# Optimization experiments

Measured on AMD Instinct MI355X. Metric: run time of the kernel, lower is better.

## Reference

```python
import jax, jax.numpy as jnp
import numpy as np

V, D, T_MAX, H, L = 96, 128, 64, 8, 4
HD = D // H          # 16
FF = 4 * D           # 512
B, T = 4096, 64
EPS = 1e-5


def setup_inputs() -> dict:
    key = jax.random.key(0)
    ks = jax.random.split(key, 24)
    n = jax.random.normal
    inp = {
        'idx': jax.random.randint(ks[0], (B, T), 0, V),
        'targets': jax.random.randint(ks[1], (B, T), 0, V),
        'tok_emb': n(ks[2], (V, D), jnp.float32) * 0.02,
        'pos_emb': n(ks[3], (T_MAX, D), jnp.float32) * 0.02,
        # per-layer stacked params; weight layout follows torch Linear [out, in]
        'Wq': n(ks[4], (L, D, D), jnp.float32) * (1.0 / np.sqrt(D)),
        'Wk': n(ks[5], (L, D, D), jnp.float32) * (1.0 / np.sqrt(D)),
        'Wv': n(ks[6], (L, D, D), jnp.float32) * (1.0 / np.sqrt(D)),
        'Wo': n(ks[7], (L, D, D), jnp.float32) * (1.0 / np.sqrt(D)),
        'bo': jnp.zeros((L, D), jnp.float32),
        'ln1_g': jnp.ones((L, D), jnp.float32),
        'ln1_b': jnp.zeros((L, D), jnp.float32),
        'ln2_g': jnp.ones((L, D), jnp.float32),
        'ln2_b': jnp.zeros((L, D), jnp.float32),
        'W1': n(ks[8], (L, FF, D), jnp.float32) * (1.0 / np.sqrt(D)),
        'b1': jnp.zeros((L, FF), jnp.float32),
        'W2': n(ks[9], (L, D, FF), jnp.float32) * (1.0 / np.sqrt(FF)),
        'b2': jnp.zeros((L, D), jnp.float32),
        'lnf_g': jnp.ones((D,), jnp.float32),
        'lnf_b': jnp.zeros((D,), jnp.float32),
        'lm_b': jnp.zeros((V,), jnp.float32),
    }
    return inp


def _layernorm(x, g, b):
    mu = jnp.mean(x, axis=-1, keepdims=True)
    var = jnp.mean(jnp.square(x - mu), axis=-1, keepdims=True)
    return (x - mu) * jax.lax.rsqrt(var + EPS) * g + b


def reference(idx, targets, tok_emb, pos_emb, Wq, Wk, Wv, Wo, bo,
              ln1_g, ln1_b, ln2_g, ln2_b, W1, b1, W2, b2,
              lnf_g, lnf_b, lm_b):
    Bc, Tc = idx.shape
    x = tok_emb[idx] + pos_emb[:Tc]                      # [B,T,D]
    causal = jnp.tril(jnp.ones((Tc, Tc), bool))
    scale = HD ** -0.5
    for l in range(L):  # small fixed layer count
        xn = _layernorm(x, ln1_g[l], ln1_b[l])
        # per-head Linears are blocks of a single [D,D] matmul
        q = (xn @ Wq[l].T).reshape(Bc, Tc, H, HD)
        k = (xn @ Wk[l].T).reshape(Bc, Tc, H, HD)
        v = (xn @ Wv[l].T).reshape(Bc, Tc, H, HD)
        wei = jnp.einsum('bqhd,bkhd->bhqk', q, k) * scale
        wei = jnp.where(causal, wei, -jnp.inf)
        wei = jax.nn.softmax(wei, axis=-1)               # dropout = identity (eval)
        att = jnp.einsum('bhqk,bkhd->bqhd', wei, v).reshape(Bc, Tc, D)
        x = x + att @ Wo[l].T + bo[l]
        xn = _layernorm(x, ln2_g[l], ln2_b[l])
        h = jax.nn.gelu(xn @ W1[l].T + b1[l], approximate=False)
        x = x + h @ W2[l].T + b2[l]
    x = _layernorm(x, lnf_g, lnf_b)
    logits = x @ tok_emb.T + lm_b                        # tied weights
    logits = logits.reshape(Bc * Tc, V)
    logp = jax.nn.log_softmax(logits, axis=-1)
    loss = -jnp.mean(jnp.take_along_axis(logp, targets.reshape(-1, 1), axis=-1))
    return logits, loss
```

## Files before the change

kernel.cpp:

```cpp
#include <hip/hip_runtime.h>
#include <hip/hip_bf16.h>
#include <math.h>

#define NTHR 512

typedef __attribute__((ext_vector_type(8))) short bf16x8;
typedef __attribute__((ext_vector_type(4))) short bf16x4;
typedef __attribute__((ext_vector_type(4))) float f32x4;

#define MFMA32(a, b, c) __builtin_amdgcn_mfma_f32_16x16x32_bf16((a), (b), (c), 0, 0, 0)

#if defined(__has_builtin)
#if __has_builtin(__builtin_amdgcn_mfma_f32_16x16x16bf16_1k)
#define HAVE_MFMA16 1
#endif
#endif
#ifdef HAVE_MFMA16
#define MFMA16(a, b, c) __builtin_amdgcn_mfma_f32_16x16x16bf16_1k((a), (b), (c), 0, 0, 0)
#else
__device__ __forceinline__ f32x4 mfma16_fb(bf16x4 a, bf16x4 b, f32x4 c) {
  asm volatile("s_nop 1\n\tv_mfma_f32_16x16x16_bf16 %0, %1, %2, %0\n\ts_nop 7\n\ts_nop 7"
               : "+v"(c) : "v"(a), "v"(b));
  return c;
}
#define MFMA16(a, b, c) mfma16_fb((a), (b), (c))
#endif

#define WS_EMB 0
#define WS_WQ  12288
#define WS_WK  (WS_WQ + 65536)
#define WS_WV  (WS_WK + 65536)
#define WS_WO  (WS_WV + 65536)
#define WS_W1  (WS_WO + 65536)
#define WS_W2  (WS_W1 + 262144)
#define WS_END (WS_W2 + 262144)

__device__ __forceinline__ short f2bf(float f) {
  union { __hip_bfloat16 h; unsigned short s; } u;
  u.h = __float2bfloat16(f);
  return (short)u.s;
}
__device__ __forceinline__ bf16x4 pk4(f32x4 v) {
  bf16x4 r;
  r[0] = f2bf(v[0]); r[1] = f2bf(v[1]); r[2] = f2bf(v[2]); r[3] = f2bf(v[3]);
  return r;
}
__device__ __forceinline__ float gelu_tanh(float x) {
  float y = x * (0.7978845608f + 0.0356774081f * x * x);
  float sg = __builtin_amdgcn_rcpf(1.f + __expf(-2.f * y));
  return x * sg;
}

__global__ void prep_weights(const float* __restrict__ tok_emb,
                             const float* __restrict__ Wq, const float* __restrict__ Wk,
                             const float* __restrict__ Wv, const float* __restrict__ Wo,
                             const float* __restrict__ W1, const float* __restrict__ W2,
                             short* __restrict__ wsb) {
  int i = blockIdx.x * NTHR + threadIdx.x;
  if (i < 12288) {
    int n = i >> 7, k = i & 127;
    wsb[WS_EMB + (k >> 3) * 768 + n * 8 + (k & 7)] = f2bf(tok_emb[i]);
    return;
  }
  i -= 12288;
  if (i < 262144) {
    int tensor = i >> 16;
    int rem = i & 65535;
    int l = rem >> 14;
    int w = rem & 16383;
    int n = w >> 7, k = w & 127;
    const float* src = tensor == 0 ? Wq : tensor == 1 ? Wk : tensor == 2 ? Wv : Wo;
    wsb[WS_WQ + tensor * 65536 + l * 16384 + (k >> 3) * 1024 + n * 8 + (k & 7)] =
        f2bf(src[rem]);
    return;
  }
  i -= 262144;
  if (i < 262144) {
    int l = i >> 16;
    int w = i & 65535;
    int n = w >> 7, k = w & 127;
    wsb[WS_W1 + l * 65536 + (k >> 3) * 4096 + n * 8 + (k & 7)] = f2bf(W1[i]);
    return;
  }
  i -= 262144;
  if (i < 262144) {
    int l = i >> 16;
    int w = i & 65535;
    int n = w >> 9, k = w & 511;
    wsb[WS_W2 + l * 65536 + (k >> 3) * 1024 + n * 8 + (k & 7)] = f2bf(W2[i]);
  }
}

__device__ __forceinline__ void layernorm(const float* __restrict__ sXl,
                                          short* __restrict__ dstl,
                                          const float* __restrict__ g,
                                          const float* __restrict__ be, int tid) {
  int r = tid >> 3, t8 = tid & 7;
  const f32x4* row = (const f32x4*)(sXl + r * 132 + t8 * 16);
  f32x4 v[4];
  float s = 0.f, s2 = 0.f;
#pragma unroll
  for (int j = 0; j < 4; ++j) {
    v[j] = row[j];
#pragma unroll
    for (int c = 0; c < 4; ++c) { s += v[j][c]; s2 += v[j][c] * v[j][c]; }
  }
  s  += __shfl_xor(s, 1, 64);  s  += __shfl_xor(s, 2, 64);  s  += __shfl_xor(s, 4, 64);
  s2 += __shfl_xor(s2, 1, 64); s2 += __shfl_xor(s2, 2, 64); s2 += __shfl_xor(s2, 4, 64);
  float mean = s * 0.0078125f;
  float rs = rsqrtf(s2 * 0.0078125f - mean * mean + 1e-5f);
  const f32x4* gp = (const f32x4*)(g + t8 * 16);
  const f32x4* bp = (const f32x4*)(be + t8 * 16);
  bf16x4* dp = (bf16x4*)(dstl + r * 136 + t8 * 16);
#pragma unroll
  for (int j = 0; j < 4; ++j) {
    f32x4 gg = gp[j], bb = bp[j], o;
#pragma unroll
    for (int c = 0; c < 4; ++c) o[c] = (v[j][c] - mean) * rs * gg[c] + bb[c];
    dp[j] = pk4(o);
  }
}

__global__ __launch_bounds__(512, 2)
void lm_forward(const int* __restrict__ idx, const int* __restrict__ targets,
                const float* __restrict__ tok_emb, const float* __restrict__ pos_emb,
                const float* __restrict__ bo, const float* __restrict__ ln1_g,
                const float* __restrict__ ln1_b, const float* __restrict__ ln2_g,
                const float* __restrict__ ln2_b, const float* __restrict__ b1,
                const float* __restrict__ b2, const float* __restrict__ lnf_g,
                const float* __restrict__ lnf_b, const float* __restrict__ lm_b,
                const short* __restrict__ wsb, float* __restrict__ out,
                float* __restrict__ loss_part) {
  __shared__ __align__(16) char smem[118016];
  float* sX  = (float*)smem;
  short* sXn = (short*)(smem + 33792);
  char*  Rg  = smem + 51200;
  short* sQ  = (short*)Rg;
  short* sK  = (short*)(Rg + 17408);
  short* sVT = (short*)(Rg + 34816);
  short* sH  = (short*)Rg;
  float* sL  = (float*)Rg;
  float* sRed = (float*)(smem + 117760);

  const int b = blockIdx.x;
  const int tid = threadIdx.x;
  const int wave = tid >> 6;
  const int lane = tid & 63;
  const int lr = lane & 15;
  const int lg = lane >> 4;
  const f32x4 fz = {0.f, 0.f, 0.f, 0.f};

#pragma unroll
  for (int k = 0; k < 4; ++k) {
    int e = (tid + k * 512) * 4;
    int t = e >> 7, d = e & 127;
    f32x4 te = *(const f32x4*)(tok_emb + idx[b * 64 + t] * 128 + d);
    f32x4 pe = *(const f32x4*)(pos_emb + e);
    *(f32x4*)(sX + t * 132 + d) = te + pe;
  }
  __syncthreads();

#pragma unroll 1
  for (int l = 0; l < 4; ++l) {
    layernorm(sX, sXn, ln1_g + l * 128, ln1_b + l * 128, tid);
    __syncthreads();

    {
      const short* wq = wsb + WS_WQ + l * 16384;
      const short* wk = wsb + WS_WK + l * 16384;
      const short* wv = wsb + WS_WV + l * 16384;
      f32x4 aq[4], ak[4], av[4];
#pragma unroll
      for (int n = 0; n < 4; ++n) { aq[n] = fz; ak[n] = fz; av[n] = fz; }
#pragma unroll
      for (int ks = 0; ks < 4; ++ks) {
        bf16x8 xf[4];
#pragma unroll
        for (int n = 0; n < 4; ++n)
          xf[n] = *(const bf16x8*)(sXn + (n * 16 + lr) * 136 + ks * 32 + lg * 8);
        int wo_ = (ks * 4 + lg) * 1024 + (wave * 16 + lr) * 8;
        bf16x8 qf = *(const bf16x8*)(wq + wo_);
        bf16x8 kf = *(const bf16x8*)(wk + wo_);
        bf16x8 vf = *(const bf16x8*)(wv + wo_);
#pragma unroll
        for (int n = 0; n < 4; ++n) {
          aq[n] = MFMA32(qf, xf[n], aq[n]);
          ak[n] = MFMA32(kf, xf[n], ak[n]);
          av[n] = MFMA32(xf[n], vf, av[n]);
        }
      }
#pragma unroll
      for (int n = 0; n < 4; ++n) {
        *(bf16x4*)(sQ + (n * 16 + lr) * 136 + wave * 16 + lg * 4) = pk4(aq[n]);
        *(bf16x4*)(sK + (n * 16 + lr) * 136 + wave * 16 + lg * 4) = pk4(ak[n]);
        *(bf16x4*)(sVT + (wave * 16 + lr) * 72 + n * 16 + lg * 4) = pk4(av[n]);
      }
    }
    __syncthreads();

    {
      const int h = wave;
      f32x4 sc[4][4];
#pragma unroll
      for (int m = 0; m < 4; ++m)
#pragma unroll
        for (int n = 0; n < 4; ++n) sc[m][n] = fz;
      bf16x4 kf[4], qf[4];
#pragma unroll
      for (int m = 0; m < 4; ++m)
        kf[m] = *(const bf16x4*)(sK + (m * 16 + lr) * 136 + h * 16 + lg * 4);
#pragma unroll
      for (int n = 0; n < 4; ++n)
        qf[n] = *(const bf16x4*)(sQ + (n * 16 + lr) * 136 + h * 16 + lg * 4);
#pragma unroll
      for (int m = 0; m < 4; ++m)
#pragma unroll
        for (int n = 0; n < 4; ++n) sc[m][n] = MFMA16(kf[m], qf[n], sc[m][n]);

      bf16x4 pf[4][4];
#pragma unroll
      for (int n = 0; n < 4; ++n) {
        int qq = n * 16 + lr;
        float mx = -1e30f;
#pragma unroll
        for (int m = 0; m < 4; ++m)
#pragma unroll
          for (int r = 0; r < 4; ++r) {
            int kk = m * 16 + lg * 4 + r;
            float s = sc[m][n][r];
            if (kk > qq) s = -1e30f;
            sc[m][n][r] = s;
            mx = fmaxf(mx, s);
          }
        mx = fmaxf(mx, __shfl_xor(mx, 16, 64));
        mx = fmaxf(mx, __shfl_xor(mx, 32, 64));
        float sum = 0.f;
#pragma unroll
        for (int m = 0; m < 4; ++m)
#pragma unroll
          for (int r = 0; r < 4; ++r) {
            float p = __expf((sc[m][n][r] - mx) * 0.25f);
            sc[m][n][r] = p;
            sum += p;
          }
        sum += __shfl_xor(sum, 16, 64);
        sum += __shfl_xor(sum, 32, 64);
        float rinv = __builtin_amdgcn_rcpf(sum);
#pragma unroll
        for (int m = 0; m < 4; ++m) {
          f32x4 pv;
#pragma unroll
          for (int r = 0; r < 4; ++r) pv[r] = sc[m][n][r] * rinv;
          pf[m][n] = pk4(pv);
        }
      }
      f32x4 ao[4];
#pragma unroll
      for (int n = 0; n < 4; ++n) ao[n] = fz;
#pragma unroll
      for (int m = 0; m < 4; ++m) {
        bf16x4 vf = *(const bf16x4*)(sVT + (h * 16 + lr) * 72 + m * 16 + lg * 4);
#pragma unroll
        for (int n = 0; n < 4; ++n) ao[n] = MFMA16(vf, pf[m][n], ao[n]);
      }
#pragma unroll
      for (int n = 0; n < 4; ++n)
        *(bf16x4*)(sXn + (n * 16 + lr) * 136 + h * 16 + lg * 4) = pk4(ao[n]);
    }
    __syncthreads();

    {
      const short* wo = wsb + WS_WO + l * 16384;
      f32x4 ac[4];
#pragma unroll
      for (int n = 0; n < 4; ++n) ac[n] = fz;
#pragma unroll
      for (int ks = 0; ks < 4; ++ks) {
        bf16x8 wf = *(const bf16x8*)(wo + (ks * 4 + lg) * 1024 + (wave * 16 + lr) * 8);
#pragma unroll
        for (int n = 0; n < 4; ++n) {
          bf16x8 bfg = *(const bf16x8*)(sXn + (n * 16 + lr) * 136 + ks * 32 + lg * 8);
          ac[n] = MFMA32(wf, bfg, ac[n]);
        }
      }
      f32x4 bo4 = *(const f32x4*)(bo + l * 128 + wave * 16 + lg * 4);
#pragma unroll
      for (int n = 0; n < 4; ++n) {
        f32x4* px = (f32x4*)(sX + (n * 16 + lr) * 132 + wave * 16 + lg * 4);
        *px = *px + ac[n] + bo4;
      }
    }
    __syncthreads();

    layernorm(sX, sXn, ln2_g + l * 128, ln2_b + l * 128, tid);
    __syncthreads();

    {
      const short* w1 = wsb + WS_W1 + l * 65536;
      const short* w2 = wsb + WS_W2 + l * 65536;
      f32x4 a1[4][4];
#pragma unroll
      for (int g = 0; g < 4; ++g)
#pragma unroll
        for (int n = 0; n < 4; ++n) a1[g][n] = fz;
#pragma unroll
      for (int ks = 0; ks < 4; ++ks) {
        bf16x8 xf[4];
#pragma unroll
        for (int n = 0; n < 4; ++n)
          xf[n] = *(const bf16x8*)(sXn + (n * 16 + lr) * 136 + ks * 32 + lg * 8);
#pragma unroll
        for (int g = 0; g < 4; ++g) {
          bf16x8 wf = *(const bf16x8*)(w1 + (ks * 4 + lg) * 4096 +
                                       (wave * 64 + g * 16 + lr) * 8);
#pragma unroll
          for (int n = 0; n < 4; ++n) a1[g][n] = MFMA32(wf, xf[n], a1[g][n]);
        }
      }
#pragma unroll
      for (int g = 0; g < 4; ++g) {
        f32x4 b1v = *(const f32x4*)(b1 + l * 512 + wave * 64 + g * 16 + lg * 4);
#pragma unroll
        for (int n = 0; n < 4; ++n) {
          f32x4 hv;
#pragma unroll
          for (int r = 0; r < 4; ++r) hv[r] = gelu_tanh(a1[g][n][r] + b1v[r]);
          *(bf16x4*)(sH + (n * 16 + lr) * 520 + wave * 64 + g * 16 + lg * 4) = pk4(hv);
        }
      }
      __syncthreads();
      f32x4 a2[4];
#pragma unroll
      for (int n = 0; n < 4; ++n) a2[n] = fz;
#pragma unroll
      for (int ks = 0; ks < 16; ++ks) {
        bf16x8 wf = *(const bf16x8*)(w2 + (ks * 4 + lg) * 1024 + (wave * 16 + lr) * 8);
#pragma unroll
        for (int n = 0; n < 4; ++n) {
          bf16x8 hf = *(const bf16x8*)(sH + (n * 16 + lr) * 520 + ks * 32 + lg * 8);
          a2[n] = MFMA32(wf, hf, a2[n]);
        }
      }
      f32x4 b2v = *(const f32x4*)(b2 + l * 128 + wave * 16 + lg * 4);
#pragma unroll
      for (int n = 0; n < 4; ++n) {
        f32x4* px = (f32x4*)(sX + (n * 16 + lr) * 132 + wave * 16 + lg * 4);
        *px = *px + a2[n] + b2v;
      }
    }
    __syncthreads();
  }

  layernorm(sX, sXn, lnf_g, lnf_b, tid);
  __syncthreads();

  if (wave < 6) {
    f32x4 al[4];
#pragma unroll
    for (int n = 0; n < 4; ++n) al[n] = fz;
#pragma unroll
    for (int ks = 0; ks < 4; ++ks) {
      bf16x8 ef = *(const bf16x8*)(wsb + WS_EMB + (ks * 4 + lg) * 768 +
                                   (wave * 16 + lr) * 8);
#pragma unroll
      for (int n = 0; n < 4; ++n) {
        bf16x8 xf = *(const bf16x8*)(sXn + (n * 16 + lr) * 136 + ks * 32 + lg * 8);
        al[n] = MFMA32(ef, xf, al[n]);
      }
    }
    f32x4 lb = *(const f32x4*)(lm_b + wave * 16 + lg * 4);
#pragma unroll
    for (int n = 0; n < 4; ++n) {
      f32x4 v = al[n] + lb;
      int token = n * 16 + lr;
      *(f32x4*)(out + ((size_t)b * 64 + token) * 96 + wave * 16 + lg * 4) = v;
      *(f32x4*)(sL + token * 100 + wave * 16 + lg * 4) = v;
    }
  }
  __syncthreads();

  {
    int r = tid >> 3, t8 = tid & 7;
    const float* lrow = sL + r * 100 + t8 * 12;
    float mx = -1e30f;
#pragma unroll
    for (int j = 0; j < 12; ++j) mx = fmaxf(mx, lrow[j]);
    mx = fmaxf(mx, __shfl_xor(mx, 1, 64));
    mx = fmaxf(mx, __shfl_xor(mx, 2, 64));
    mx = fmaxf(mx, __shfl_xor(mx, 4, 64));
    float sum = 0.f;
#pragma unroll
    for (int j = 0; j < 12; ++j) sum += __expf(lrow[j] - mx);
    sum += __shfl_xor(sum, 1, 64);
    sum += __shfl_xor(sum, 2, 64);
    sum += __shfl_xor(sum, 4, 64);
    if (t8 == 0) {
      float lse = logf(sum) + mx;
      sRed[r] = lse - sL[r * 100 + targets[b * 64 + r]];
    }
  }
  __syncthreads();
  if (wave == 0) {
    float v = sRed[lane];
#pragma unroll
    for (int m = 32; m >= 1; m >>= 1) v += __shfl_xor(v, m, 64);
    if (lane == 0) loss_part[b] = v;
  }
}

__global__ void loss_reduce(const float* __restrict__ loss_part, float* __restrict__ out_loss) {
  __shared__ float red[256];
  int t = threadIdx.x;
  float s = 0.f;
  for (int i = t; i < 4096; i += 256) s += loss_part[i];
  red[t] = s;
  __syncthreads();
  for (int k = 128; k >= 1; k >>= 1) {
    if (t < k) red[t] += red[t + k];
    __syncthreads();
  }
  if (t == 0) out_loss[0] = red[0] * (1.f / 262144.f);
}

extern "C" void kernel_launch(void* const* d_in, const int* in_sizes, int n_in,
                              void* d_out, int out_size, void* d_ws, size_t ws_size,
                              hipStream_t stream) {
  (void)in_sizes; (void)n_in; (void)ws_size;
  const int* idx      = (const int*)d_in[0];
  const int* targets  = (const int*)d_in[1];
  const float* tok_emb = (const float*)d_in[2];
  const float* pos_emb = (const float*)d_in[3];
  const float* Wq = (const float*)d_in[4];
  const float* Wk = (const float*)d_in[5];
  const float* Wv = (const float*)d_in[6];
  const float* Wo = (const float*)d_in[7];
  const float* bo = (const float*)d_in[8];
  const float* ln1_g = (const float*)d_in[9];
  const float* ln1_b = (const float*)d_in[10];
  const float* ln2_g = (const float*)d_in[11];
  const float* ln2_b = (const float*)d_in[12];
  const float* W1 = (const float*)d_in[13];
  const float* b1 = (const float*)d_in[14];
  const float* W2 = (const float*)d_in[15];
  const float* b2 = (const float*)d_in[16];
  const float* lnf_g = (const float*)d_in[17];
  const float* lnf_b = (const float*)d_in[18];
  const float* lm_b = (const float*)d_in[19];

  short* wsb = (short*)d_ws;
  float* loss_part = (float*)((char*)d_ws + (size_t)WS_END * 2);
  float* out = (float*)d_out;

  prep_weights<<<1560, NTHR, 0, stream>>>(tok_emb, Wq, Wk, Wv, Wo, W1, W2, wsb);
  lm_forward<<<4096, NTHR, 0, stream>>>(idx, targets, tok_emb, pos_emb, bo,
                                        ln1_g, ln1_b, ln2_g, ln2_b, b1, b2,
                                        lnf_g, lnf_b, lm_b, wsb, out, loss_part);
  loss_reduce<<<1, 256, 0, stream>>>(loss_part, out + (out_size - 1));
}
```

Measured before the change: 880.1 us.

## Keep residual stream in registers, shrink LDS, fuse attention per wave

Moves the residual stream x out of LDS and into per-lane registers. LayerNorm becomes a cross-wave partial-sum reduction through a small LDS buffer. Q/K/V stay in registers and each wave runs its head's attention directly with causal block skipping, and the MLP hidden layer is split into two 256-wide chunks to halve the sH buffer. Together these cut LDS use substantially, so launch bounds can ask for four blocks per CU, and several barriers and LDS round-trips go away. The trade-off is higher register pressure and extra barriers inside the LayerNorm reduction.

Measured after the change: 1.030 ms. 1.17x slower.

```diff
diff --git a/kernel.cpp b/kernel.cpp
--- a/kernel.cpp
+++ b/kernel.cpp
@@ -45,10 +45,9 @@
   r[0] = f2bf(v[0]); r[1] = f2bf(v[1]); r[2] = f2bf(v[2]); r[3] = f2bf(v[3]);
   return r;
 }
-__device__ __forceinline__ float gelu_tanh(float x) {
-  float y = x * (0.7978845608f + 0.0356774081f * x * x);
-  float sg = __builtin_amdgcn_rcpf(1.f + __expf(-2.f * y));
-  return x * sg;
+__device__ __forceinline__ float gelu1(float x) {
+  float y = x * __builtin_fmaf(0.0356774081f, x * x, 0.7978845608f);
+  return x * __builtin_amdgcn_rcpf(1.f + exp2f(-2.885390082f * y));
 }
 
 __global__ void prep_weights(const float* __restrict__ tok_emb,
@@ -91,37 +90,52 @@
   }
 }
 
-__device__ __forceinline__ void layernorm(const float* __restrict__ sXl,
-                                          short* __restrict__ dstl,
-                                          const float* __restrict__ g,
-                                          const float* __restrict__ be, int tid) {
-  int r = tid >> 3, t8 = tid & 7;
-  const f32x4* row = (const f32x4*)(sXl + r * 132 + t8 * 16);
-  f32x4 v[4];
-  float s = 0.f, s2 = 0.f;
-#pragma unroll
-  for (int j = 0; j < 4; ++j) {
-    v[j] = row[j];
-#pragma unroll
-    for (int c = 0; c < 4; ++c) { s += v[j][c]; s2 += v[j][c] * v[j][c]; }
-  }
-  s  += __shfl_xor(s, 1, 64);  s  += __shfl_xor(s, 2, 64);  s  += __shfl_xor(s, 4, 64);
-  s2 += __shfl_xor(s2, 1, 64); s2 += __shfl_xor(s2, 2, 64); s2 += __shfl_xor(s2, 4, 64);
-  float mean = s * 0.0078125f;
-  float rs = rsqrtf(s2 * 0.0078125f - mean * mean + 1e-5f);
-  const f32x4* gp = (const f32x4*)(g + t8 * 16);
-  const f32x4* bp = (const f32x4*)(be + t8 * 16);
-  bf16x4* dp = (bf16x4*)(dstl + r * 136 + t8 * 16);
-#pragma unroll
-  for (int j = 0; j < 4; ++j) {
-    f32x4 gg = gp[j], bb = bp[j], o;
-#pragma unroll
-    for (int c = 0; c < 4; ++c) o[c] = (v[j][c] - mean) * rs * gg[c] + bb[c];
-    dp[j] = pk4(o);
-  }
-}
-
-__global__ __launch_bounds__(512, 2)
+__device__ __forceinline__ void ln_regs(const f32x4* x, const float* __restrict__ g,
+                                        const float* __restrict__ bb,
+                                        short* __restrict__ sXn, float* __restrict__ sPart,
+                                        int wave, int lr, int lg) {
+  float s[4], s2[4];
+#pragma unroll
+  for (int n = 0; n < 4; ++n) {
+    s[n] = (x[n][0] + x[n][1]) + (x[n][2] + x[n][3]);
+    s2[n] = (x[n][0] * x[n][0] + x[n][1] * x[n][1]) +
+            (x[n][2] * x[n][2] + x[n][3] * x[n][3]);
+  }
+#pragma unroll
+  for (int n = 0; n < 4; ++n) {
+    s[n] += __shfl_xor(s[n], 16, 64);  s[n] += __shfl_xor(s[n], 32, 64);
+    s2[n] += __shfl_xor(s2[n], 16, 64); s2[n] += __shfl_xor(s2[n], 32, 64);
+  }
+  if (lg == 0) {
+#pragma unroll
+    for (int n = 0; n < 4; ++n) {
+      float2 p; p.x = s[n]; p.y = s2[n];
+      *(float2*)(sPart + (wave * 64 + 16 * n + lr) * 2) = p;
+    }
+  }
+  __syncthreads();
+  int dbase = wave * 16 + lg * 4;
+  f32x4 g4 = *(const f32x4*)(g + dbase);
+  f32x4 b4 = *(const f32x4*)(bb + dbase);
+#pragma unroll
+  for (int n = 0; n < 4; ++n) {
+    float S = 0.f, S2 = 0.f;
+#pragma unroll
+    for (int w = 0; w < 8; ++w) {
+      float2 p = *(const float2*)(sPart + (w * 64 + 16 * n + lr) * 2);
+      S += p.x; S2 += p.y;
+    }
+    float mean = S * 0.0078125f;
+    float rstd = rsqrtf(__builtin_fmaf(-mean, mean, S2 * 0.0078125f) + 1e-5f);
+    f32x4 o;
+#pragma unroll
+    for (int c = 0; c < 4; ++c) o[c] = __builtin_fmaf((x[n][c] - mean) * rstd, g4[c], b4[c]);
+    *(bf16x4*)(sXn + (16 * n + lr) * 136 + dbase) = pk4(o);
+  }
+  __syncthreads();
+}
+
+__global__ __launch_bounds__(512, 4)
 void lm_forward(const int* __restrict__ idx, const int* __restrict__ targets,
                 const float* __restrict__ tok_emb, const float* __restrict__ pos_emb,
                 const float* __restrict__ bo, const float* __restrict__ ln1_g,
@@ -131,16 +145,11 @@
                 const float* __restrict__ lnf_b, const float* __restrict__ lm_b,
                 const short* __restrict__ wsb, float* __restrict__ out,
                 float* __restrict__ loss_part) {
-  __shared__ __align__(16) char smem[118016];
-  float* sX  = (float*)smem;
-  short* sXn = (short*)(smem + 33792);
-  char*  Rg  = smem + 51200;
-  short* sQ  = (short*)Rg;
-  short* sK  = (short*)(Rg + 17408);
-  short* sVT = (short*)(Rg + 34816);
-  short* sH  = (short*)Rg;
-  float* sL  = (float*)Rg;
-  float* sRed = (float*)(smem + 117760);
+  __shared__ __align__(16) short sXn[64 * 136];
+  __shared__ __align__(16) short sH[64 * 264];
+  __shared__ __align__(16) float sPart[8 * 64 * 2];
+  __shared__ float sTgt[64];
+  short* sAtt = sH;
 
   const int b = blockIdx.x;
   const int tid = threadIdx.x;
@@ -148,124 +157,106 @@
   const int lane = tid & 63;
   const int lr = lane & 15;
   const int lg = lane >> 4;
+  const int dbase = wave * 16 + lg * 4;
   const f32x4 fz = {0.f, 0.f, 0.f, 0.f};
-
-#pragma unroll
-  for (int k = 0; k < 4; ++k) {
-    int e = (tid + k * 512) * 4;
-    int t = e >> 7, d = e & 127;
-    f32x4 te = *(const f32x4*)(tok_emb + idx[b * 64 + t] * 128 + d);
-    f32x4 pe = *(const f32x4*)(pos_emb + e);
-    *(f32x4*)(sX + t * 132 + d) = te + pe;
-  }
-  __syncthreads();
+  const float KSC = 0.360673760f;
+
+  f32x4 x[4];
+#pragma unroll
+  for (int n = 0; n < 4; ++n) {
+    int t = 16 * n + lr;
+    int tk = idx[b * 64 + t];
+    f32x4 te = *(const f32x4*)(tok_emb + tk * 128 + dbase);
+    f32x4 pe = *(const f32x4*)(pos_emb + t * 128 + dbase);
+    x[n] = te + pe;
+  }
 
 #pragma unroll 1
   for (int l = 0; l < 4; ++l) {
-    layernorm(sX, sXn, ln1_g + l * 128, ln1_b + l * 128, tid);
-    __syncthreads();
-
+    ln_regs(x, ln1_g + l * 128, ln1_b + l * 128, sXn, sPart, wave, lr, lg);
+
+    const short* wq = wsb + WS_WQ + l * 16384;
+    const short* wk = wsb + WS_WK + l * 16384;
+    const short* wv = wsb + WS_WV + l * 16384;
+    bf16x4 qf[4], kf[4], vf[4];
     {
-      const short* wq = wsb + WS_WQ + l * 16384;
-      const short* wk = wsb + WS_WK + l * 16384;
-      const short* wv = wsb + WS_WV + l * 16384;
-      f32x4 aq[4], ak[4], av[4];
-#pragma unroll
-      for (int n = 0; n < 4; ++n) { aq[n] = fz; ak[n] = fz; av[n] = fz; }
+      f32x4 aq[4], ak[4];
+#pragma unroll
+      for (int n = 0; n < 4; ++n) { aq[n] = fz; ak[n] = fz; }
 #pragma unroll
       for (int ks = 0; ks < 4; ++ks) {
         bf16x8 xf[4];
 #pragma unroll
         for (int n = 0; n < 4; ++n)
-          xf[n] = *(const bf16x8*)(sXn + (n * 16 + lr) * 136 + ks * 32 + lg * 8);
+          xf[n] = *(const bf16x8*)(sXn + (16 * n + lr) * 136 + ks * 32 + lg * 8);
         int wo_ = (ks * 4 + lg) * 1024 + (wave * 16 + lr) * 8;
-        bf16x8 qf = *(const bf16x8*)(wq + wo_);
-        bf16x8 kf = *(const bf16x8*)(wk + wo_);
-        bf16x8 vf = *(const bf16x8*)(wv + wo_);
+        bf16x8 qw = *(const bf16x8*)(wq + wo_);
+        bf16x8 kw = *(const bf16x8*)(wk + wo_);
 #pragma unroll
         for (int n = 0; n < 4; ++n) {
-          aq[n] = MFMA32(qf, xf[n], aq[n]);
-          ak[n] = MFMA32(kf, xf[n], ak[n]);
-          av[n] = MFMA32(xf[n], vf, av[n]);
-        }
-      }
-#pragma unroll
-      for (int n = 0; n < 4; ++n) {
-        *(bf16x4*)(sQ + (n * 16 + lr) * 136 + wave * 16 + lg * 4) = pk4(aq[n]);
-        *(bf16x4*)(sK + (n * 16 + lr) * 136 + wave * 16 + lg * 4) = pk4(ak[n]);
-        *(bf16x4*)(sVT + (wave * 16 + lr) * 72 + n * 16 + lg * 4) = pk4(av[n]);
-      }
-    }
-    __syncthreads();
-
+          aq[n] = MFMA32(qw, xf[n], aq[n]);
+          ak[n] = MFMA32(kw, xf[n], ak[n]);
+        }
+      }
+#pragma unroll
+      for (int n = 0; n < 4; ++n) { qf[n] = pk4(aq[n] * KSC); kf[n] = pk4(ak[n]); }
+    }
     {
-      const int h = wave;
-      f32x4 sc[4][4];
+      f32x4 av[4];
+#pragma unroll
+      for (int n = 0; n < 4; ++n) av[n] = fz;
+#pragma unroll
+      for (int ks = 0; ks < 4; ++ks) {
+        bf16x8 xf[4];
+#pragma unroll
+        for (int n = 0; n < 4; ++n)
+          xf[n] = *(const bf16x8*)(sXn + (16 * n + lr) * 136 + ks * 32 + lg * 8);
+        bf16x8 vw = *(const bf16x8*)(wv + (ks * 4 + lg) * 1024 + (wave * 16 + lr) * 8);
+#pragma unroll
+        for (int n = 0; n < 4; ++n) av[n] = MFMA32(xf[n], vw, av[n]);
+      }
+#pragma unroll
+      for (int m = 0; m < 4; ++m) vf[m] = pk4(av[m]);
+    }
+
+#pragma unroll
+    for (int n = 0; n < 4; ++n) {
+      f32x4 sc[4];
 #pragma unroll
       for (int m = 0; m < 4; ++m)
-#pragma unroll
-        for (int n = 0; n < 4; ++n) sc[m][n] = fz;
-      bf16x4 kf[4], qf[4];
+        if (m <= n) sc[m] = MFMA16(kf[m], qf[n], fz);
+#pragma unroll
+      for (int r = 0; r < 4; ++r)
+        if (lg * 4 + r > lr) sc[n][r] = -1e30f;
+      float mx = -1e30f;
 #pragma unroll
       for (int m = 0; m < 4; ++m)
-        kf[m] = *(const bf16x4*)(sK + (m * 16 + lr) * 136 + h * 16 + lg * 4);
-#pragma unroll
-      for (int n = 0; n < 4; ++n)
-        qf[n] = *(const bf16x4*)(sQ + (n * 16 + lr) * 136 + h * 16 + lg * 4);
+        if (m <= n)
+#pragma unroll
+          for (int r = 0; r < 4; ++r) mx = fmaxf(mx, sc[m][r]);
+      mx = fmaxf(mx, __shfl_xor(mx, 16, 64));
+      mx = fmaxf(mx, __shfl_xor(mx, 32, 64));
+      float sum = 0.f;
 #pragma unroll
       for (int m = 0; m < 4; ++m)
-#pragma unroll
-        for (int n = 0; n < 4; ++n) sc[m][n] = MFMA16(kf[m], qf[n], sc[m][n]);
-
-      bf16x4 pf[4][4];
-#pragma unroll
-      for (int n = 0; n < 4; ++n) {
-        int qq = n * 16 + lr;
-        float mx = -1e30f;
-#pragma unroll
-        for (int m = 0; m < 4; ++m)
+        if (m <= n)
 #pragma unroll
           for (int r = 0; r < 4; ++r) {
-            int kk = m * 16 + lg * 4 + r;
-            float s = sc[m][n][r];
-            if (kk > qq) s = -1e30f;
-            sc[m][n][r] = s;
-            mx = fmaxf(mx, s);
-          }
-        mx = fmaxf(mx, __shfl_xor(mx, 16, 64));
-        mx = fmaxf(mx, __shfl_xor(mx, 32, 64));
-        float sum = 0.f;
-#pragma unroll
-        for (int m = 0; m < 4; ++m)
-#pragma unroll
-          for (int r = 0; r < 4; ++r) {
-            float p = __expf((sc[m][n][r] - mx) * 0.25f);
-            sc[m][n][r] = p;
+            float p = exp2f(sc[m][r] - mx);
+            sc[m][r] = p;
             sum += p;
           }
-        sum += __shfl_xor(sum, 16, 64);
-        sum += __shfl_xor(sum, 32, 64);
-        float rinv = __builtin_amdgcn_rcpf(sum);
-#pragma unroll
-        for (int m = 0; m < 4; ++m) {
-          f32x4 pv;
-#pragma unroll
-          for (int r = 0; r < 4; ++r) pv[r] = sc[m][n][r] * rinv;
-          pf[m][n] = pk4(pv);
-        }
-      }
-      f32x4 ao[4];
-#pragma unroll
-      for (int n = 0; n < 4; ++n) ao[n] = fz;
-#pragma unroll
-      for (int m = 0; m < 4; ++m) {
-        bf16x4 vf = *(const bf16x4*)(sVT + (h * 16 + lr) * 72 + m * 16 + lg * 4);
-#pragma unroll
-        for (int n = 0; n < 4; ++n) ao[n] = MFMA16(vf, pf[m][n], ao[n]);
-      }
-#pragma unroll
-      for (int n = 0; n < 4; ++n)
-        *(bf16x4*)(sXn + (n * 16 + lr) * 136 + h * 16 + lg * 4) = pk4(ao[n]);
+      sum += __shfl_xor(sum, 16, 64);
+      sum += __shfl_xor(sum, 32, 64);
+      float rinv = __builtin_amdgcn_rcpf(sum);
+      f32x4 ao = fz;
+#pragma unroll
+      for (int m = 0; m < 4; ++m)
+        if (m <= n) {
+          bf16x4 pf = pk4(sc[m] * rinv);
+          ao = MFMA16(vf[m], pf, ao);
+        }
+      *(bf16x4*)(sAtt + (16 * n + lr) * 136 + dbase) = pk4(ao);
     }
     __syncthreads();
 
@@ -279,80 +270,77 @@
         bf16x8 wf = *(const bf16x8*)(wo + (ks * 4 + lg) * 1024 + (wave * 16 + lr) * 8);
 #pragma unroll
         for (int n = 0; n < 4; ++n) {
-          bf16x8 bfg = *(const bf16x8*)(sXn + (n * 16 + lr) * 136 + ks * 32 + lg * 8);
-          ac[n] = MFMA32(wf, bfg, ac[n]);
-        }
-      }
-      f32x4 bo4 = *(const f32x4*)(bo + l * 128 + wave * 16 + lg * 4);
-#pragma unroll
-      for (int n = 0; n < 4; ++n) {
-        f32x4* px = (f32x4*)(sX + (n * 16 + lr) * 132 + wave * 16 + lg * 4);
-        *px = *px + ac[n] + bo4;
-      }
-    }
-    __syncthreads();
-
-    layernorm(sX, sXn, ln2_g + l * 128, ln2_b + l * 128, tid);
-    __syncthreads();
+          bf16x8 af = *(const bf16x8*)(sAtt + (16 * n + lr) * 136 + ks * 32 + lg * 8);
+          ac[n] = MFMA32(wf, af, ac[n]);
+        }
+      }
+      f32x4 bo4 = *(const f32x4*)(bo + l * 128 + dbase);
+#pragma unroll
+      for (int n = 0; n < 4; ++n) x[n] = x[n] + ac[n] + bo4;
+    }
+
+    ln_regs(x, ln2_g + l * 128, ln2_b + l * 128, sXn, sPart, wave, lr, lg);
 
     {
       const short* w1 = wsb + WS_W1 + l * 65536;
       const short* w2 = wsb + WS_W2 + l * 65536;
-      f32x4 a1[4][4];
-#pragma unroll
-      for (int g = 0; g < 4; ++g)
-#pragma unroll
-        for (int n = 0; n < 4; ++n) a1[g][n] = fz;
-#pragma unroll
-      for (int ks = 0; ks < 4; ++ks) {
-        bf16x8 xf[4];
-#pragma unroll
-        for (int n = 0; n < 4; ++n)
-          xf[n] = *(const bf16x8*)(sXn + (n * 16 + lr) * 136 + ks * 32 + lg * 8);
-#pragma unroll
-        for (int g = 0; g < 4; ++g) {
-          bf16x8 wf = *(const bf16x8*)(w1 + (ks * 4 + lg) * 4096 +
-                                       (wave * 64 + g * 16 + lr) * 8);
-#pragma unroll
-          for (int n = 0; n < 4; ++n) a1[g][n] = MFMA32(wf, xf[n], a1[g][n]);
-        }
-      }
-#pragma unroll
-      for (int g = 0; g < 4; ++g) {
-        f32x4 b1v = *(const f32x4*)(b1 + l * 512 + wave * 64 + g * 16 + lg * 4);
-#pragma unroll
-        for (int n = 0; n < 4; ++n) {
-          f32x4 hv;
-#pragma unroll
-          for (int r = 0; r < 4; ++r) hv[r] = gelu_tanh(a1[g][n][r] + b1v[r]);
-          *(bf16x4*)(sH + (n * 16 + lr) * 520 + wave * 64 + g * 16 + lg * 4) = pk4(hv);
-        }
-      }
-      __syncthreads();
       f32x4 a2[4];
 #pragma unroll
       for (int n = 0; n < 4; ++n) a2[n] = fz;
-#pragma unroll
-      for (int ks = 0; ks < 16; ++ks) {
-        bf16x8 wf = *(const bf16x8*)(w2 + (ks * 4 + lg) * 1024 + (wave * 16 + lr) * 8);
-#pragma unroll
-        for (int n = 0; n < 4; ++n) {
-          bf16x8 hf = *(const bf16x8*)(sH + (n * 16 + lr) * 520 + ks * 32 + lg * 8);
-          a2[n] = MFMA32(wf, hf, a2[n]);
-        }
-      }
-      f32x4 b2v = *(const f32x4*)(b2 + l * 128 + wave * 16 + lg * 4);
-#pragma unroll
-      for (int n = 0; n < 4; ++n) {
-        f32x4* px = (f32x4*)(sX + (n * 16 + lr) * 132 + wave * 16 + lg * 4);
-        *px = *px + a2[n] + b2v;
-      }
-    }
-    __syncthreads();
-  }
-
-  layernorm(sX, sXn, lnf_g, lnf_b, tid);
-  __syncthreads();
+#pragma unroll 1
+      for (int c = 0; c < 2; ++c) {
+        f32x4 a1[2][4];
+#pragma unroll
+        for (int g = 0; g < 2; ++g)
+#pragma unroll
+          for (int n = 0; n < 4; ++n) a1[g][n] = fz;
+#pragma unroll
+        for (int ks = 0; ks < 4; ++ks) {
+          bf16x8 xf[4];
+#pragma unroll
+          for (int n = 0; n < 4; ++n)
+            xf[n] = *(const bf16x8*)(sXn + (16 * n + lr) * 136 + ks * 32 + lg * 8);
+          bf16x8 w1f0 = *(const bf16x8*)(w1 + (ks * 4 + lg) * 4096 +
+                                         (c * 256 + wave * 32 + lr) * 8);
+          bf16x8 w1f1 = *(const bf16x8*)(w1 + (ks * 4 + lg) * 4096 +
+                                         (c * 256 + wave * 32 + 16 + lr) * 8);
+#pragma unroll
+          for (int n = 0; n < 4; ++n) {
+            a1[0][n] = MFMA32(w1f0, xf[n], a1[0][n]);
+            a1[1][n] = MFMA32(w1f1, xf[n], a1[1][n]);
+          }
+        }
+#pragma unroll
+        for (int g = 0; g < 2; ++g) {
+          f32x4 b1v = *(const f32x4*)(b1 + l * 512 + c * 256 + wave * 32 + g * 16 + lg * 4);
+#pragma unroll
+          for (int n = 0; n < 4; ++n) {
+            f32x4 hv;
+#pragma unroll
+            for (int r = 0; r < 4; ++r) hv[r] = gelu1(a1[g][n][r] + b1v[r]);
+            *(bf16x4*)(sH + (16 * n + lr) * 264 + wave * 32 + g * 16 + lg * 4) = pk4(hv);
+          }
+        }
+        __syncthreads();
+#pragma unroll
+        for (int ks = 0; ks < 8; ++ks) {
+          bf16x8 w2f = *(const bf16x8*)(w2 + (c * 32 + ks * 4 + lg) * 1024 +
+                                        (wave * 16 + lr) * 8);
+#pragma unroll
+          for (int n = 0; n < 4; ++n) {
+            bf16x8 hf = *(const bf16x8*)(sH + (16 * n + lr) * 264 + ks * 32 + lg * 8);
+            a2[n] = MFMA32(w2f, hf, a2[n]);
+          }
+        }
+        if (c == 0) __syncthreads();
+      }
+      f32x4 b2v = *(const f32x4*)(b2 + l * 128 + dbase);
+#pragma unroll
+      for (int n = 0; n < 4; ++n) x[n] = x[n] + a2[n] + b2v;
+    }
+  }
+
+  ln_regs(x, lnf_g, lnf_b, sXn, sPart, wave, lr, lg);
 
   if (wave < 6) {
     f32x4 al[4];
@@ -364,47 +352,53 @@
                                    (wave * 16 + lr) * 8);
 #pragma unroll
       for (int n = 0; n < 4; ++n) {
-        bf16x8 xf = *(const bf16x8*)(sXn + (n * 16 + lr) * 136 + ks * 32 + lg * 8);
+        bf16x8 xf = *(const bf16x8*)(sXn + (16 * n + lr) * 136 + ks * 32 + lg * 8);
         al[n] = MFMA32(ef, xf, al[n]);
       }
     }
-    f32x4 lb = *(const f32x4*)(lm_b + wave * 16 + lg * 4);
+    f32x4 lb = *(const f32x4*)(lm_b + dbase);
 #pragma unroll
     for (int n = 0; n < 4; ++n) {
+      int t = 16 * n + lr;
       f32x4 v = al[n] + lb;
-      int token = n * 16 + lr;
-      *(f32x4*)(out + ((size_t)b * 64 + token) * 96 + wave * 16 + lg * 4) = v;
-      *(f32x4*)(sL + token * 100 + wave * 16 + lg * 4) = v;
-    }
-  }
-  __syncthreads();
-
-  {
-    int r = tid >> 3, t8 = tid & 7;
-    const float* lrow = sL + r * 100 + t8 * 12;
-    float mx = -1e30f;
-#pragma unroll
-    for (int j = 0; j < 12; ++j) mx = fmaxf(mx, lrow[j]);
-    mx = fmaxf(mx, __shfl_xor(mx, 1, 64));
-    mx = fmaxf(mx, __shfl_xor(mx, 2, 64));
-    mx = fmaxf(mx, __shfl_xor(mx, 4, 64));
-    float sum = 0.f;
-#pragma unroll
-    for (int j = 0; j < 12; ++j) sum += __expf(lrow[j] - mx);
-    sum += __shfl_xor(sum, 1, 64);
-    sum += __shfl_xor(sum, 2, 64);
-    sum += __shfl_xor(sum, 4, 64);
-    if (t8 == 0) {
-      float lse = logf(sum) + mx;
-      sRed[r] = lse - sL[r * 100 + targets[b * 64 + r]];
+      *(f32x4*)(out + ((size_t)b * 64 + t) * 96 + dbase) = v;
+      float mx = fmaxf(fmaxf(v[0], v[1]), fmaxf(v[2], v[3]));
+      mx = fmaxf(mx, __shfl_xor(mx, 16, 64));
+      mx = fmaxf(mx, __shfl_xor(mx, 32, 64));
+      float es = __expf(v[0] - mx) + __expf(v[1] - mx) +
+                 __expf(v[2] - mx) + __expf(v[3] - mx);
+      es += __shfl_xor(es, 16, 64);
+      es += __shfl_xor(es, 32, 64);
+      if (lg == 0) {
+        float2 p; p.x = mx; p.y = es;
+        *(float2*)(sPart + (wave * 64 + t) * 2) = p;
+      }
+      int cgt = targets[b * 64 + t];
+      if ((cgt >> 4) == wave && ((cgt >> 2) & 3) == lg) {
+#pragma unroll
+        for (int r = 0; r < 4; ++r)
+          if ((cgt & 3) == r) sTgt[t] = v[r];
+      }
     }
   }
   __syncthreads();
   if (wave == 0) {
-    float v = sRed[lane];
-#pragma unroll
-    for (int m = 32; m >= 1; m >>= 1) v += __shfl_xor(v, m, 64);
-    if (lane == 0) loss_part[b] = v;
+    float mxw[6], esw[6];
+#pragma unroll
+    for (int w = 0; w < 6; ++w) {
+      float2 p = *(const float2*)(sPart + (w * 64 + lane) * 2);
+      mxw[w] = p.x; esw[w] = p.y;
+    }
+    float MX = mxw[0];
+#pragma unroll
+    for (int w = 1; w < 6; ++w) MX = fmaxf(MX, mxw[w]);
+    float SUM = 0.f;
+#pragma unroll
+    for (int w = 0; w < 6; ++w) SUM += esw[w] * __expf(mxw[w] - MX);
+    float lt = MX + logf(SUM) - sTgt[lane];
+#pragma unroll
+    for (int m = 32; m >= 1; m >>= 1) lt += __shfl_xor(lt, m, 64);
+    if (lane == 0) loss_part[b] = lt;
   }
 }
 
```

## Swizzle LDS layouts, skip masked attention tiles, fold softmax scale into Q

Applied to the files above, without the earlier changes.

Replaces padded row strides for the normalized activations and FFN hidden buffer with an XOR-swizzled layout, which removes padding and is meant to avoid LDS bank conflicts on the MFMA operand loads. Attention now computes only the causal lower-triangular score tiles, masks only the diagonal tiles, and fuses the P·V product into the per-query-block softmax loop. The softmax scale and log2(e) are folded into Q so the softmax can use exp2, and GELU also switches to exp2 with an FMA. Q/K/V strides change to 140/76, and V is transposed with scalar stores, which may add store cost or new bank conflicts.

Measured after the change: 1.185 ms. +34.6%, slower.

```diff
diff --git a/kernel.cpp b/kernel.cpp
--- a/kernel.cpp
+++ b/kernel.cpp
@@ -45,10 +45,16 @@
   r[0] = f2bf(v[0]); r[1] = f2bf(v[1]); r[2] = f2bf(v[2]); r[3] = f2bf(v[3]);
   return r;
 }
-__device__ __forceinline__ float gelu_tanh(float x) {
-  float y = x * (0.7978845608f + 0.0356774081f * x * x);
-  float sg = __builtin_amdgcn_rcpf(1.f + __expf(-2.f * y));
-  return x * sg;
+__device__ __forceinline__ float gelu1(float x) {
+  float y = x * __builtin_fmaf(0.0356774081f, x * x, 0.7978845608f);
+  return x * __builtin_amdgcn_rcpf(1.f + exp2f(-2.885390082f * y));
+}
+
+__device__ __forceinline__ int xn_idx(int r, int col) {
+  return r * 128 + ((((col >> 3) ^ (r & 7))) << 3) + (col & 7);
+}
+__device__ __forceinline__ int h_idx(int r, int col) {
+  return r * 512 + ((((col >> 3) ^ (r & 7))) << 3) + (col & 7);
 }
 
 __global__ void prep_weights(const float* __restrict__ tok_emb,
@@ -111,13 +117,12 @@
   float rs = rsqrtf(s2 * 0.0078125f - mean * mean + 1e-5f);
   const f32x4* gp = (const f32x4*)(g + t8 * 16);
   const f32x4* bp = (const f32x4*)(be + t8 * 16);
-  bf16x4* dp = (bf16x4*)(dstl + r * 136 + t8 * 16);
 #pragma unroll
   for (int j = 0; j < 4; ++j) {
     f32x4 gg = gp[j], bb = bp[j], o;
 #pragma unroll
     for (int c = 0; c < 4; ++c) o[c] = (v[j][c] - mean) * rs * gg[c] + bb[c];
-    dp[j] = pk4(o);
+    *(bf16x4*)(dstl + xn_idx(r, t8 * 16 + j * 4)) = pk4(o);
   }
 }
 
@@ -131,16 +136,16 @@
                 const float* __restrict__ lnf_b, const float* __restrict__ lm_b,
                 const short* __restrict__ wsb, float* __restrict__ out,
                 float* __restrict__ loss_part) {
-  __shared__ __align__(16) char smem[118016];
+  __shared__ __align__(16) char smem[115968];
   float* sX  = (float*)smem;
   short* sXn = (short*)(smem + 33792);
-  char*  Rg  = smem + 51200;
+  char*  Rg  = smem + 50176;
   short* sQ  = (short*)Rg;
-  short* sK  = (short*)(Rg + 17408);
-  short* sVT = (short*)(Rg + 34816);
+  short* sK  = (short*)(Rg + 17920);
+  short* sVT = (short*)(Rg + 35840);
   short* sH  = (short*)Rg;
   float* sL  = (float*)Rg;
-  float* sRed = (float*)(smem + 117760);
+  float* sRed = (float*)(smem + 115712);
 
   const int b = blockIdx.x;
   const int tid = threadIdx.x;
@@ -149,6 +154,7 @@
   const int lr = lane & 15;
   const int lg = lane >> 4;
   const f32x4 fz = {0.f, 0.f, 0.f, 0.f};
+  const float KSC = 0.360673760f;
 
 #pragma unroll
   for (int k = 0; k < 4; ++k) {
@@ -177,95 +183,80 @@
         bf16x8 xf[4];
 #pragma unroll
         for (int n = 0; n < 4; ++n)
-          xf[n] = *(const bf16x8*)(sXn + (n * 16 + lr) * 136 + ks * 32 + lg * 8);
+          xf[n] = *(const bf16x8*)(sXn + xn_idx(16 * n + lr, ks * 32 + lg * 8));
         int wo_ = (ks * 4 + lg) * 1024 + (wave * 16 + lr) * 8;
-        bf16x8 qf = *(const bf16x8*)(wq + wo_);
-        bf16x8 kf = *(const bf16x8*)(wk + wo_);
-        bf16x8 vf = *(const bf16x8*)(wv + wo_);
+        bf16x8 qw = *(const bf16x8*)(wq + wo_);
+        bf16x8 kw = *(const bf16x8*)(wk + wo_);
+        bf16x8 vw = *(const bf16x8*)(wv + wo_);
 #pragma unroll
         for (int n = 0; n < 4; ++n) {
-          aq[n] = MFMA32(qf, xf[n], aq[n]);
-          ak[n] = MFMA32(kf, xf[n], ak[n]);
-          av[n] = MFMA32(xf[n], vf, av[n]);
+          aq[n] = MFMA32(qw, xf[n], aq[n]);
+          ak[n] = MFMA32(kw, xf[n], ak[n]);
+          av[n] = MFMA32(xf[n], vw, av[n]);
         }
       }
 #pragma unroll
       for (int n = 0; n < 4; ++n) {
-        *(bf16x4*)(sQ + (n * 16 + lr) * 136 + wave * 16 + lg * 4) = pk4(aq[n]);
-        *(bf16x4*)(sK + (n * 16 + lr) * 136 + wave * 16 + lg * 4) = pk4(ak[n]);
-        *(bf16x4*)(sVT + (wave * 16 + lr) * 72 + n * 16 + lg * 4) = pk4(av[n]);
+        *(bf16x4*)(sQ + (n * 16 + lr) * 140 + wave * 16 + lg * 4) = pk4(aq[n] * KSC);
+        *(bf16x4*)(sK + (n * 16 + lr) * 140 + wave * 16 + lg * 4) = pk4(ak[n]);
+        bf16x4 vv = pk4(av[n]);
+        int col = wave * 16 + lr;
+#pragma unroll
+        for (int r = 0; r < 4; ++r)
+          sVT[col * 76 + n * 16 + lg * 4 + r] = vv[r];
       }
     }
     __syncthreads();
 
     {
       const int h = wave;
+      bf16x4 kf[4], qf[4], vfr[4];
+#pragma unroll
+      for (int m = 0; m < 4; ++m) {
+        kf[m] = *(const bf16x4*)(sK + (m * 16 + lr) * 140 + h * 16 + lg * 4);
+        vfr[m] = *(const bf16x4*)(sVT + (h * 16 + lr) * 76 + m * 16 + lg * 4);
+      }
+#pragma unroll
+      for (int n = 0; n < 4; ++n)
+        qf[n] = *(const bf16x4*)(sQ + (n * 16 + lr) * 140 + h * 16 + lg * 4);
       f32x4 sc[4][4];
 #pragma unroll
-      for (int m = 0; m < 4; ++m)
-#pragma unroll
-        for (int n = 0; n < 4; ++n) sc[m][n] = fz;
-      bf16x4 kf[4], qf[4];
-#pragma unroll
-      for (int m = 0; m < 4; ++m)
-        kf[m] = *(const bf16x4*)(sK + (m * 16 + lr) * 136 + h * 16 + lg * 4);
-#pragma unroll
       for (int n = 0; n < 4; ++n)
-        qf[n] = *(const bf16x4*)(sQ + (n * 16 + lr) * 136 + h * 16 + lg * 4);
-#pragma unroll
-      for (int m = 0; m < 4; ++m)
-#pragma unroll
-        for (int n = 0; n < 4; ++n) sc[m][n] = MFMA16(kf[m], qf[n], sc[m][n]);
-
-      bf16x4 pf[4][4];
+#pragma unroll
+        for (int m = 0; m <= n; ++m)
+          sc[m][n] = MFMA16(kf[m], qf[n], fz);
 #pragma unroll
       for (int n = 0; n < 4; ++n) {
-        int qq = n * 16 + lr;
+#pragma unroll
+        for (int r = 0; r < 4; ++r)
+          if (lg * 4 + r > lr) sc[n][n][r] = -1e30f;
         float mx = -1e30f;
 #pragma unroll
-        for (int m = 0; m < 4; ++m)
-#pragma unroll
-          for (int r = 0; r < 4; ++r) {
-            int kk = m * 16 + lg * 4 + r;
-            float s = sc[m][n][r];
-            if (kk > qq) s = -1e30f;
-            sc[m][n][r] = s;
-            mx = fmaxf(mx, s);
-          }
+        for (int m = 0; m <= n; ++m)
+#pragma unroll
+          for (int r = 0; r < 4; ++r) mx = fmaxf(mx, sc[m][n][r]);
         mx = fmaxf(mx, __shfl_xor(mx, 16, 64));
         mx = fmaxf(mx, __shfl_xor(mx, 32, 64));
         float sum = 0.f;
 #pragma unroll
-        for (int m = 0; m < 4; ++m)
+        for (int m = 0; m <= n; ++m)
 #pragma unroll
           for (int r = 0; r < 4; ++r) {
-            float p = __expf((sc[m][n][r] - mx) * 0.25f);
+            float p = exp2f(sc[m][n][r] - mx);
             sc[m][n][r] = p;
             sum += p;
           }
         sum += __shfl_xor(sum, 16, 64);
         sum += __shfl_xor(sum, 32, 64);
         float rinv = __builtin_amdgcn_rcpf(sum);
-#pragma unroll
-        for (int m = 0; m < 4; ++m) {
-          f32x4 pv;
-#pragma unroll
-          for (int r = 0; r < 4; ++r) pv[r] = sc[m][n][r] * rinv;
-          pf[m][n] = pk4(pv);
-        }
-      }
-      f32x4 ao[4];
-#pragma unroll
-      for (int n = 0; n < 4; ++n) ao[n] = fz;
-#pragma unroll
-      for (int m = 0; m < 4; ++m) {
-        bf16x4 vf = *(const bf16x4*)(sVT + (h * 16 + lr) * 72 + m * 16 + lg * 4);
-#pragma unroll
-        for (int n = 0; n < 4; ++n) ao[n] = MFMA16(vf, pf[m][n], ao[n]);
-      }
-#pragma unroll
-      for (int n = 0; n < 4; ++n)
-        *(bf16x4*)(sXn + (n * 16 + lr) * 136 + h * 16 + lg * 4) = pk4(ao[n]);
+        f32x4 ao = fz;
+#pragma unroll
+        for (int m = 0; m <= n; ++m) {
+          bf16x4 pf = pk4(sc[m][n] * rinv);
+          ao = MFMA16(vfr[m], pf, ao);
+        }
+        *(bf16x4*)(sXn + xn_idx(16 * n + lr, h * 16 + lg * 4)) = pk4(ao);
+      }
     }
     __syncthreads();
 
@@ -279,8 +270,8 @@
         bf16x8 wf = *(const bf16x8*)(wo + (ks * 4 + lg) * 1024 + (wave * 16 + lr) * 8);
 #pragma unroll
         for (int n = 0; n < 4; ++n) {
-          bf16x8 bfg = *(const bf16x8*)(sXn + (n * 16 + lr) * 136 + ks * 32 + lg * 8);
-          ac[n] = MFMA32(wf, bfg, ac[n]);
+          bf16x8 af = *(const bf16x8*)(sXn + xn_idx(16 * n + lr, ks * 32 + lg * 8));
+          ac[n] = MFMA32(wf, af, ac[n]);
         }
       }
       f32x4 bo4 = *(const f32x4*)(bo + l * 128 + wave * 16 + lg * 4);
@@ -308,7 +299,7 @@
         bf16x8 xf[4];
 #pragma unroll
         for (int n = 0; n < 4; ++n)
-          xf[n] = *(const bf16x8*)(sXn + (n * 16 + lr) * 136 + ks * 32 + lg * 8);
+          xf[n] = *(const bf16x8*)(sXn + xn_idx(16 * n + lr, ks * 32 + lg * 8));
 #pragma unroll
         for (int g = 0; g < 4; ++g) {
           bf16x8 wf = *(const bf16x8*)(w1 + (ks * 4 + lg) * 4096 +
@@ -324,8 +315,8 @@
         for (int n = 0; n < 4; ++n) {
           f32x4 hv;
 #pragma unroll
-          for (int r = 0; r < 4; ++r) hv[r] = gelu_tanh(a1[g][n][r] + b1v[r]);
-          *(bf16x4*)(sH + (n * 16 + lr) * 520 + wave * 64 + g * 16 + lg * 4) = pk4(hv);
+          for (int r = 0; r < 4; ++r) hv[r] = gelu1(a1[g][n][r] + b1v[r]);
+          *(bf16x4*)(sH + h_idx(16 * n + lr, wave * 64 + g * 16 + lg * 4)) = pk4(hv);
         }
       }
       __syncthreads();
@@ -337,7 +328,7 @@
         bf16x8 wf = *(const bf16x8*)(w2 + (ks * 4 + lg) * 1024 + (wave * 16 + lr) * 8);
 #pragma unroll
         for (int n = 0; n < 4; ++n) {
-          bf16x8 hf = *(const bf16x8*)(sH + (n * 16 + lr) * 520 + ks * 32 + lg * 8);
+          bf16x8 hf = *(const bf16x8*)(sH + h_idx(16 * n + lr, ks * 32 + lg * 8));
           a2[n] = MFMA32(wf, hf, a2[n]);
         }
       }
@@ -364,7 +355,7 @@
                                    (wave * 16 + lr) * 8);
 #pragma unroll
       for (int n = 0; n < 4; ++n) {
-        bf16x8 xf = *(const bf16x8*)(sXn + (n * 16 + lr) * 136 + ks * 32 + lg * 8);
+        bf16x8 xf = *(const bf16x8*)(sXn + xn_idx(16 * n + lr, ks * 32 + lg * 8));
         al[n] = MFMA32(ef, xf, al[n]);
       }
     }
```
